# Kernel tuning notes

Measured on AMD Instinct MI355X. Metric: run time of the kernel, lower is better.

The kernel has to match this reference:

```python
import jax, jax.numpy as jnp
from jax import lax
import numpy as np

B, T, H = 128, 512, 512  # batch, seq_length, hidden_dim (== input_dim)


def _xavier(key, shape):
    fan_in, fan_out = shape[1], shape[0]
    limit = float(np.sqrt(6.0 / (fan_in + fan_out)))
    return jax.random.uniform(key, shape, jnp.float32, -limit, limit)


def setup_inputs() -> dict:
    key = jax.random.key(0)
    ks = jax.random.split(key, 10)
    s = 1.0 / np.sqrt(H)  # torch LSTM default init range
    return {
        "x": jax.random.normal(ks[0], (B, T, H), jnp.float32),
        "W_ih": jax.random.uniform(ks[1], (4 * H, H), jnp.float32, -s, s),
        "W_hh": jax.random.uniform(ks[2], (4 * H, H), jnp.float32, -s, s),
        "b_ih": jax.random.uniform(ks[3], (4 * H,), jnp.float32, -s, s),
        "b_hh": jax.random.uniform(ks[4], (4 * H,), jnp.float32, -s, s),
        "Ve": _xavier(ks[5], (1, H)),
        "U1": _xavier(ks[6], (H, 2 * H)),
        "U2": _xavier(ks[7], (H, H)),
        "W_out": _xavier(ks[8], (2, H)),
        "b_out": jnp.zeros((2,), jnp.float32),
    }


def _lstm(x, W_ih, W_hh, b_ih, b_hh):
    # x: [B, T, D] -> hidden states [B, T, H]; PyTorch gate order i,f,g,o
    b = b_ih + b_hh
    # precompute input projections for all timesteps: [T, B, 4H]
    xg = jnp.einsum('btd,gd->tbg', x, W_ih) + b

    def step(carry, xt):
        h, c = carry
        g = xt + h @ W_hh.T  # [B, 4H]
        i, f, gg, o = jnp.split(g, 4, axis=1)
        c = jax.nn.sigmoid(f) * c + jax.nn.sigmoid(i) * jnp.tanh(gg)
        h = jax.nn.sigmoid(o) * jnp.tanh(c)
        return (h, c), h

    h0 = jnp.zeros((x.shape[0], W_hh.shape[1]), x.dtype)
    (_, _), hs = lax.scan(step, (h0, h0), xg)
    return jnp.swapaxes(hs, 0, 1)  # [B, T, H]


def reference(x, W_ih, W_hh, b_ih, b_hh, Ve, U1, U2, W_out, b_out):
    h = _lstm(x, W_ih, W_hh, b_ih, b_hh)  # [B, T, H]
    h_last = h[:, -1, :]  # [B, H]
    # additive attention, vectorized over all timesteps
    Hdim = h.shape[-1]
    u1 = jnp.einsum('bth,gh->btg', h, U1[:, :Hdim]) + jnp.einsum('bh,gh->bg', h_last, U1[:, Hdim:])[:, None, :]
    u2 = jnp.einsum('btd,gd->btg', x, U2)
    u = jnp.tanh(u1 + u2)  # [B, T, H]
    e = jnp.einsum('bth,h->bt', u, Ve[0])
    alpha = jax.nn.softmax(e, axis=1)  # [B, T]
    context = jnp.einsum('bt,bth->bh', alpha, h)  # [B, H]
    params = context @ W_out.T + b_out  # [B, 2]
    mu = params[:, 0]
    sigma = jax.nn.softplus(params[:, 1]) + 1e-5
    return (mu, sigma)
```

## Files before the change

### kernel.cpp

```cpp
#include <hip/hip_runtime.h>
#include <stdint.h>


using short8  = __attribute__((ext_vector_type(8))) short;
using short4v = __attribute__((ext_vector_type(4))) short;
using floatx4 = __attribute__((ext_vector_type(4))) float;

#define MFMA16(a, b, c) __builtin_amdgcn_mfma_f32_16x16x32_bf16((a), (b), (c), 0, 0, 0)

__device__ __forceinline__ unsigned short f2b(float f) {
    unsigned u = __float_as_uint(f);
    u += 0x7FFFu + ((u >> 16) & 1u);
    return (unsigned short)(u >> 16);
}
__device__ __forceinline__ float b2f(unsigned short h) {
    return __uint_as_float(((unsigned)h) << 16);
}
__device__ __forceinline__ float sigm(float x) { return 1.0f / (1.0f + __expf(-x)); }
__device__ __forceinline__ float tanh_(float x) { return 1.0f - 2.0f / (__expf(2.0f * x) + 1.0f); }

__global__ __launch_bounds__(256) void prep(
    const float* __restrict__ x, const float* __restrict__ Wih, const float* __restrict__ Whh,
    const float* __restrict__ bih, const float* __restrict__ bhh,
    const float* __restrict__ U1, const float* __restrict__ U2,
    unsigned short* __restrict__ x_bf, unsigned short* __restrict__ Wih_bf,
    unsigned short* __restrict__ Whh_bf, unsigned short* __restrict__ U1a,
    unsigned short* __restrict__ U1b, unsigned short* __restrict__ U2b,
    float* __restrict__ bias)
{
    const long long NX4 = 33554432LL / 4;
    const long long NREST = 1048576LL + 1048576LL + 524288LL + 262144LL + 2048LL;
    const long long total = NX4 + NREST;
    for (long long u = (long long)blockIdx.x * 256 + threadIdx.x; u < total;
         u += (long long)gridDim.x * 256) {
        if (u < NX4) {
            float4 v = ((const float4*)x)[u];
            short4v o;
            o[0] = (short)f2b(v.x); o[1] = (short)f2b(v.y);
            o[2] = (short)f2b(v.z); o[3] = (short)f2b(v.w);
            *(short4v*)&x_bf[u * 4] = o;
        } else {
            long long i = u - NX4;
            if (i < 1048576) { Wih_bf[i] = f2b(Wih[i]); continue; }
            i -= 1048576;
            if (i < 1048576) { Whh_bf[i] = f2b(Whh[i]); continue; }
            i -= 1048576;
            if (i < 524288) {
                int row = (int)(i >> 10), col = (int)(i & 1023);
                if (col < 512) U1a[row * 512 + col] = f2b(U1[i]);
                else           U1b[row * 512 + (col - 512)] = f2b(U1[i]);
                continue;
            }
            i -= 524288;
            if (i < 262144) { U2b[i] = f2b(U2[i]); continue; }
            i -= 262144;
            bias[i] = bih[i] + bhh[i];
        }
    }
}

__device__ __forceinline__ void gemm_core_t(
    const unsigned short* __restrict__ A, long long lda,
    const unsigned short* __restrict__ Bm,
    unsigned short* __restrict__ C,
    const float* __restrict__ bias,
    int n0, int tfix, int tid, unsigned short* sbuf)
{
    unsigned short* At = sbuf;
    unsigned short* Bt = sbuf + 128 * 72;
    unsigned short* Ct = sbuf;

    const int wv = tid >> 6, lane = tid & 63, l15 = lane & 15, q = lane >> 4;
    const int wm = wv & 1, wn = wv >> 1;

    floatx4 acc[4][4];
    for (int i = 0; i < 4; i++)
        for (int j = 0; j < 4; j++) acc[i][j] = (floatx4){0.f, 0.f, 0.f, 0.f};

    for (int k0 = 0; k0 < 512; k0 += 64) {
        for (int p = 0; p < 4; p++) {
            int idx = tid + p * 256;
            int row = idx >> 3, ch = idx & 7;
            *(short8*)&At[row * 72 + ch * 8] =
                *(const short8*)&A[(long long)row * lda + k0 + ch * 8];
            *(short8*)&Bt[row * 72 + ch * 8] =
                *(const short8*)&Bm[(long long)(n0 + row) * 512 + k0 + ch * 8];
        }
        __syncthreads();
        for (int ks = 0; ks < 64; ks += 32) {
            short8 af[4], bfv[4];
            for (int mi = 0; mi < 4; mi++)
                af[mi] = *(const short8*)&At[(wm * 64 + mi * 16 + l15) * 72 + ks + q * 8];
            for (int ni = 0; ni < 4; ni++)
                bfv[ni] = *(const short8*)&Bt[(wn * 64 + ni * 16 + l15) * 72 + ks + q * 8];
            for (int mi = 0; mi < 4; mi++)
                for (int ni = 0; ni < 4; ni++)
                    acc[mi][ni] = MFMA16(af[mi], bfv[ni], acc[mi][ni]);
        }
        __syncthreads();
    }

    float bv[4];
    for (int ni = 0; ni < 4; ni++)
        bv[ni] = bias[n0 + wn * 64 + ni * 16 + l15];

    for (int mi = 0; mi < 4; mi++)
        for (int ni = 0; ni < 4; ni++)
            for (int r = 0; r < 4; r++)
                Ct[(wm * 64 + mi * 16 + q * 4 + r) * 128 + wn * 64 + ni * 16 + l15] =
                    f2b(acc[mi][ni][r] + bv[ni]);
    __syncthreads();

    for (int p = 0; p < 8; p++) {
        int idx = tid + p * 256;
        int row = idx >> 4, ch = idx & 15;
        int n = n0 + ch * 8;
        int gate = n >> 9, jg = (n >> 4) & 31, c0 = gate * 16 + (n & 15);
        long long dst = (((long long)tfix * 32 + jg) * 128 + row) * 64 + c0;
        *(short8*)&C[dst] = *(const short8*)&Ct[row * 128 + ch * 8];
    }
}

template<int NNI>
__device__ __forceinline__ void attn_helper_body(
    const unsigned short* __restrict__ h_all,
    const unsigned short* __restrict__ x_bf,
    const unsigned short* __restrict__ U1a,
    const unsigned short* __restrict__ U2b,
    unsigned short* __restrict__ xg_out,
    int* __restrict__ syncp,
    int b, int t0, int nBase, int tid, char* smem)
{
    const int bg = b >> 4;
    if (tid < 8) {
        while (__hip_atomic_load(&syncp[16 + (bg * 8 + tid) * 16],
                                 __ATOMIC_RELAXED,
                                 __HIP_MEMORY_SCOPE_AGENT) < t0 + 32)
            __builtin_amdgcn_s_sleep(8);
    }
    __syncthreads();

    unsigned short* Bt2 = (unsigned short*)smem;
    unsigned short* At2 = (unsigned short*)smem + (NNI * 64) * 40;

    const int wv = tid >> 6, lane = tid & 63, l15 = lane & 15, q = lane >> 4;

    floatx4 acc[2][NNI];
    #pragma unroll
    for (int mi = 0; mi < 2; mi++)
        #pragma unroll
        for (int ni = 0; ni < NNI; ni++) acc[mi][ni] = (floatx4){0.f, 0.f, 0.f, 0.f};

    for (int it = 0; it < 32; it++) {
        const int phase = it >> 4, kk = (it & 15) * 32;
        const unsigned short* Bsrc = phase ? U2b : U1a;
        __syncthreads();
        #pragma unroll
        for (int pp = 0; pp < NNI; pp++) {
            int idx = tid + pp * 256;
            int row = idx >> 2, ch = idx & 3;
            *(short8*)&Bt2[row * 40 + ch * 8] =
                *(const short8*)&Bsrc[(long long)(nBase + row) * 512 + kk + ch * 8];
        }
        if (tid < 128) {
            int row = tid >> 2, ch = tid & 3;
            if (phase == 0) {
                unsigned long long* p = (unsigned long long*)
                    &h_all[((long long)b * 512 + t0 + row) * 512 + kk + ch * 8];
                unsigned long long lo = __hip_atomic_load(p, __ATOMIC_RELAXED,
                                                          __HIP_MEMORY_SCOPE_AGENT);
                unsigned long long hi = __hip_atomic_load(p + 1, __ATOMIC_RELAXED,
                                                          __HIP_MEMORY_SCOPE_AGENT);
                unsigned long long* d = (unsigned long long*)&At2[row * 40 + ch * 8];
                d[0] = lo; d[1] = hi;
            } else {
                *(short8*)&At2[row * 40 + ch * 8] =
                    *(const short8*)&x_bf[((long long)b * 512 + t0 + row) * 512 + kk + ch * 8];
            }
        }
        __syncthreads();
        short8 af0 = *(const short8*)&At2[(l15) * 40 + q * 8];
        short8 af1 = *(const short8*)&At2[(16 + l15) * 40 + q * 8];
        #pragma unroll
        for (int ni = 0; ni < NNI; ni++) {
            short8 bfv = *(const short8*)&Bt2[(wv * (NNI * 16) + ni * 16 + l15) * 40 + q * 8];
            acc[0][ni] = MFMA16(af0, bfv, acc[0][ni]);
            acc[1][ni] = MFMA16(af1, bfv, acc[1][ni]);
        }
    }
    #pragma unroll
    for (int mi = 0; mi < 2; mi++)
        #pragma unroll
        for (int ni = 0; ni < NNI; ni++) {
            const int n = nBase + wv * (NNI * 16) + ni * 16 + l15;
            #pragma unroll
            for (int r = 0; r < 4; r++) {
                const int t = t0 + mi * 16 + q * 4 + r;
                float* slot = (float*)&xg_out[(((long long)t * 32 + (n >> 5)) * 128 + b) * 64];
                slot[n & 31] = acc[mi][ni][r];
            }
        }
}

#define GEMM_WGS 8192
#define ATTN_WGS 2432
__global__ __launch_bounds__(256, 1) void mega(
    const unsigned short* __restrict__ xg,
    const unsigned short* __restrict__ Whh,
    unsigned short* __restrict__ h_all,
    unsigned int* __restrict__ ring,
    const unsigned short* __restrict__ x_bf,
    const unsigned short* __restrict__ Wih_bf,
    const float* __restrict__ bias,
    unsigned short* __restrict__ xg_out,
    int* __restrict__ syncp,
    const unsigned short* __restrict__ U1a,
    const unsigned short* __restrict__ U2b)
{
    __shared__ __align__(16) char smem[86016];

    const int tid = threadIdx.x;

    if (blockIdx.x >= 64 && blockIdx.x < 64 + GEMM_WGS) {
        int g = blockIdx.x - 64;
        int t = g >> 4;
        int n0 = (g & 15) << 7;
        gemm_core_t(x_bf + (long long)t * 512, 512LL * 512, Wih_bf,
                    xg_out, bias, n0, t, tid, (unsigned short*)smem);
        __syncthreads();
        if (tid == 0)
            __hip_atomic_fetch_add(&syncp[1088 + t], 1, __ATOMIC_RELEASE,
                                   __HIP_MEMORY_SCOPE_AGENT);
        return;
    }

    if (blockIdx.x >= 64 + GEMM_WGS) {
        const int g = blockIdx.x - 64 - GEMM_WGS;
        if (g < 1920) {
            attn_helper_body<8>(h_all, x_bf, U1a, U2b, xg_out, syncp,
                                g & 127, (g >> 7) * 32, 0, tid, smem);
        } else {
            const int j = g - 1920;
            attn_helper_body<2>(h_all, x_bf, U1a, U2b, xg_out, syncp,
                                j & 127, 480, (j >> 7) * 128, tid, smem);
        }
        return;
    }

    unsigned int (*At)[16 * 264] = (unsigned int (*)[16 * 264])smem;

    const int wv = tid >> 6, lane = tid & 63, l15 = lane & 15, q = lane >> 4;
    const int bg = blockIdx.x >> 3, jgb = blockIdx.x & 7;
    const int b0 = bg * 16;
    const int jg32 = jgb * 4 + wv;
    const int hid = jg32 * 16 + l15;

    short8 Wreg[4][16];
    #pragma unroll
    for (int ct = 0; ct < 4; ct++)
        #pragma unroll
        for (int kk = 0; kk < 16; kk++)
            Wreg[ct][kk] = *(const short8*)
                &Whh[(long long)(ct * 512 + hid) * 512 + kk * 32 + q * 8];

    float cst[4] = {0.f, 0.f, 0.f, 0.f};

    for (int t = 0; t < 512; t++) {
        if ((t & 15) == 0) {
            if (tid < 16) {
                while (__hip_atomic_load(&syncp[1088 + t + tid], __ATOMIC_ACQUIRE,
                                         __HIP_MEMORY_SCOPE_AGENT) < 16)
                    __builtin_amdgcn_s_sleep(8);
            }
            __syncthreads();
        }
        const long long xbase = ((long long)(t * 32 + jg32) * 128 + b0) * 64;
        floatx4 acc[4];
        #pragma unroll
        for (int ct = 0; ct < 4; ct++)
            #pragma unroll
            for (int r = 0; r < 4; r++)
                acc[ct][r] = b2f(xg[xbase + (q * 4 + r) * 64 + ct * 16 + l15]);

        if (t > 0) {
            const unsigned want = (unsigned)(t - 1);
            const int sl = (t - 1) & 1;
            unsigned long long* rb = (unsigned long long*)
                (ring + sl * 65536 + b0 * 512);
            unsigned long long w[16];
            #pragma unroll
            for (int i = 0; i < 16; i++)
                w[i] = __hip_atomic_load(&rb[tid + i * 256], __ATOMIC_RELAXED,
                                         __HIP_MEMORY_SCOPE_AGENT);
            while (true) {
                unsigned bad = 0;
                #pragma unroll
                for (int i = 0; i < 16; i++) {
                    unsigned lo = (unsigned)(w[i] >> 16) & 0xFFFFu;
                    unsigned hi = (unsigned)(w[i] >> 48);
                    bad |= (lo ^ want) | (hi ^ want);
                }
                if (!bad) break;
                #pragma unroll
                for (int i = 0; i < 16; i++) {
                    unsigned lo = (unsigned)(w[i] >> 16) & 0xFFFFu;
                    unsigned hi = (unsigned)(w[i] >> 48);
                    if ((lo ^ want) | (hi ^ want))
                        w[i] = __hip_atomic_load(&rb[tid + i * 256], __ATOMIC_RELAXED,
                                                 __HIP_MEMORY_SCOPE_AGENT);
                }
            }
            unsigned int* dst = &At[sl][0];
            #pragma unroll
            for (int i = 0; i < 16; i++) {
                int idx = tid + i * 256;
                int row = idx >> 8, k = idx & 255;
                dst[row * 264 + k] =
                    (unsigned)(w[i] & 0xFFFFu) | ((unsigned)(w[i] >> 32) << 16);
            }
            __syncthreads();
            const unsigned int* ap = &At[sl][l15 * 264 + q * 4];
            #pragma unroll
            for (int kk = 0; kk < 16; kk++) {
                short8 af = *(const short8*)(ap + kk * 16);
                acc[0] = MFMA16(af, Wreg[0][kk], acc[0]);
                acc[1] = MFMA16(af, Wreg[1][kk], acc[1]);
                acc[2] = MFMA16(af, Wreg[2][kk], acc[2]);
                acc[3] = MFMA16(af, Wreg[3][kk], acc[3]);
            }
        }
        unsigned short hbv[4];
        #pragma unroll
        for (int r = 0; r < 4; r++) {
            float ig = sigm(acc[0][r]);
            float fg = sigm(acc[1][r]);
            float gv = tanh_(acc[2][r]);
            float og = sigm(acc[3][r]);
            cst[r] = fg * cst[r] + ig * gv;
            hbv[r] = f2b(og * tanh_(cst[r]));
        }
        #pragma unroll
        for (int r = 0; r < 4; r++) {
            const int b = b0 + q * 4 + r;
            __hip_atomic_store(&ring[(t & 1) * 65536 + b * 512 + hid],
                               ((unsigned)t << 16) | hbv[r], __ATOMIC_RELAXED,
                               __HIP_MEMORY_SCOPE_AGENT);
        }
        #pragma unroll
        for (int r = 0; r < 4; r++) {
            const int b = b0 + q * 4 + r;
            int o = __shfl_xor((int)hbv[r], 1);
            if (!(l15 & 1)) {
                unsigned v = (unsigned)hbv[r] | (((unsigned)(unsigned short)o) << 16);
                __hip_atomic_store(
                    (unsigned*)&h_all[(long long)b * 262144 + (long long)t * 512 + hid],
                    v, __ATOMIC_RELAXED, __HIP_MEMORY_SCOPE_AGENT);
            }
        }
        if ((t & 15) == 15) {
            __syncthreads();
            if (tid == 0)
                __hip_atomic_store(&syncp[16 + (int)blockIdx.x * 16], t + 1,
                                   __ATOMIC_RELAXED, __HIP_MEMORY_SCOPE_AGENT);
        }
    }
}

__global__ __launch_bounds__(256) void attn_out(
    const unsigned short* __restrict__ a_xg,
    const unsigned short* __restrict__ h_all,
    const unsigned short* __restrict__ U1b,
    const float* __restrict__ Ve,
    const float* __restrict__ Wout, const float* __restrict__ bout,
    float* __restrict__ outp)
{
    __shared__ float hl[512];
    __shared__ float u1s[512];
    __shared__ float se[512];
    __shared__ float sm[512];
    __shared__ float red[8];
    const int b = blockIdx.x, tid = threadIdx.x;
    const int wv = tid >> 6, lane = tid & 63;

    {
        unsigned v = ((const unsigned*)(h_all + (long long)b * 262144 + 511LL * 512))[tid];
        hl[2 * tid]     = b2f((unsigned short)(v & 0xFFFFu));
        hl[2 * tid + 1] = b2f((unsigned short)(v >> 16));
    }
    __syncthreads();
    #pragma unroll
    for (int rr = 0; rr < 2; rr++) {
        const int n = tid + rr * 256;
        const unsigned short* up = &U1b[(long long)n * 512];
        float s = 0.f;
        for (int k = 0; k < 512; k += 8) {
            short8 v8 = *(const short8*)&up[k];
            #pragma unroll
            for (int j = 0; j < 8; j++)
                s += hl[k + j] * b2f((unsigned short)v8[j]);
        }
        u1s[n] = s;
    }
    __syncthreads();

    const int n0 = lane * 8;
    float ve[8], ub[8];
    #pragma unroll
    for (int j = 0; j < 8; j++) {
        ve[j] = Ve[n0 + j];
        ub[j] = u1s[n0 + j];
    }
    for (int it = 0; it < 64; it++) {
        const int t = it * 8 + wv * 2;
        const float* s0p = (const float*)
            &a_xg[(((long long)t * 32 + (n0 >> 5)) * 128 + b) * 64];
        const float* s1p = (const float*)
            &a_xg[(((long long)(t + 1) * 32 + (n0 >> 5)) * 128 + b) * 64];
        float4 a0 = *(const float4*)&s0p[n0 & 31];
        float4 a1 = *(const float4*)&s0p[(n0 & 31) + 4];
        float4 a2 = *(const float4*)&s1p[n0 & 31];
        float4 a3 = *(const float4*)&s1p[(n0 & 31) + 4];
        float s0 = ve[0] * tanh_(a0.x + ub[0]) + ve[1] * tanh_(a0.y + ub[1])
                 + ve[2] * tanh_(a0.z + ub[2]) + ve[3] * tanh_(a0.w + ub[3])
                 + ve[4] * tanh_(a1.x + ub[4]) + ve[5] * tanh_(a1.y + ub[5])
                 + ve[6] * tanh_(a1.z + ub[6]) + ve[7] * tanh_(a1.w + ub[7]);
        float s1 = ve[0] * tanh_(a2.x + ub[0]) + ve[1] * tanh_(a2.y + ub[1])
                 + ve[2] * tanh_(a2.z + ub[2]) + ve[3] * tanh_(a2.w + ub[3])
                 + ve[4] * tanh_(a3.x + ub[4]) + ve[5] * tanh_(a3.y + ub[5])
                 + ve[6] * tanh_(a3.z + ub[6]) + ve[7] * tanh_(a3.w + ub[7]);
        #pragma unroll
        for (int off = 1; off <= 32; off <<= 1) {
            s0 += __shfl_xor(s0, off);
            s1 += __shfl_xor(s1, off);
        }
        if (lane == 0) { se[t] = s0; se[t + 1] = s1; }
    }
    __syncthreads();

    float e0 = se[tid], e1 = se[256 + tid];
    float mx = fmaxf(e0, e1);
    for (int off = 32; off; off >>= 1) mx = fmaxf(mx, __shfl_xor(mx, off));
    if (lane == 0) red[wv] = mx;
    __syncthreads();
    mx = fmaxf(fmaxf(red[0], red[1]), fmaxf(red[2], red[3]));

    float s0 = __expf(e0 - mx), s1 = __expf(e1 - mx);
    sm[tid] = s0; sm[256 + tid] = s1;
    float ss = s0 + s1;
    for (int off = 32; off; off >>= 1) ss += __shfl_xor(ss, off);
    if (lane == 0) red[4 + wv] = ss;
    __syncthreads();
    float inv = 1.0f / (red[4] + red[5] + red[6] + red[7]);

    const unsigned int* hp = (const unsigned int*)(h_all + (long long)b * 262144);
    float a0 = 0.f, a1 = 0.f;
    for (int t = 0; t < 512; t += 4) {
        #pragma unroll
        for (int j = 0; j < 4; j++) {
            float al = sm[t + j];
            unsigned v = hp[(t + j) * 256 + tid];
            a0 += al * b2f((unsigned short)(v & 0xFFFFu));
            a1 += al * b2f((unsigned short)(v >> 16));
        }
    }
    a0 *= inv; a1 *= inv;

    float q0 = a0 * Wout[2 * tid] + a1 * Wout[2 * tid + 1];
    float q1 = a0 * Wout[512 + 2 * tid] + a1 * Wout[512 + 2 * tid + 1];
    for (int off = 32; off; off >>= 1) { q0 += __shfl_xor(q0, off); q1 += __shfl_xor(q1, off); }
    __syncthreads();
    if (lane == 0) { red[wv] = q0; red[4 + wv] = q1; }
    __syncthreads();
    if (tid == 0) {
        float P0 = red[0] + red[1] + red[2] + red[3] + bout[0];
        float P1 = red[4] + red[5] + red[6] + red[7] + bout[1];
        outp[b] = P0;
        float sp = (P1 > 15.0f) ? P1 : log1pf(__expf(P1));
        outp[128 + b] = sp + 1e-5f;
    }
}

extern "C" void kernel_launch(void* const* d_in, const int* in_sizes, int n_in,
                              void* d_out, int out_size, void* d_ws, size_t ws_size,
                              hipStream_t stream)
{
    const float* x    = (const float*)d_in[0];
    const float* Wih  = (const float*)d_in[1];
    const float* Whh  = (const float*)d_in[2];
    const float* bih  = (const float*)d_in[3];
    const float* bhh  = (const float*)d_in[4];
    const float* Ve   = (const float*)d_in[5];
    const float* U1   = (const float*)d_in[6];
    const float* U2   = (const float*)d_in[7];
    const float* Wout = (const float*)d_in[8];
    const float* bout = (const float*)d_in[9];
    float* out = (float*)d_out;

    char* ws = (char*)d_ws;
    size_t off = 0;
    auto alloc = [&](size_t bytes) -> void* {
        void* p = ws + off;
        off += (bytes + 255) & ~(size_t)255;
        return p;
    };
    unsigned short* x_bf   = (unsigned short*)alloc(33554432ull * 2);
    unsigned short* Wih_bf = (unsigned short*)alloc(1048576ull * 2);
    unsigned short* Whh_bf = (unsigned short*)alloc(1048576ull * 2);
    unsigned short* U1a    = (unsigned short*)alloc(262144ull * 2);
    unsigned short* U1b    = (unsigned short*)alloc(262144ull * 2);
    unsigned short* U2b    = (unsigned short*)alloc(262144ull * 2);
    float*          bias   = (float*)alloc(2048ull * 4);
    unsigned short* xg     = (unsigned short*)alloc(134217728ull * 2);
    unsigned short* h_all  = (unsigned short*)alloc(33554432ull * 2);
    unsigned int*   ring   = (unsigned int*)alloc(131072ull * 4);
    int*            syncp  = (int*)alloc(8192ull);
    if (off > ws_size) return;

    hipMemsetAsync(syncp, 0, 8192, stream);
    prep<<<4096, 256, 0, stream>>>(x, Wih, Whh, bih, bhh, U1, U2,
                                   x_bf, Wih_bf, Whh_bf, U1a, U1b, U2b, bias);
    mega<<<64 + GEMM_WGS + ATTN_WGS, 256, 0, stream>>>(
        xg, Whh_bf, h_all, ring, x_bf, Wih_bf, bias, xg, syncp, U1a, U2b);
    attn_out<<<128, 256, 0, stream>>>(xg, h_all, U1b, Ve, Wout, bout, out);
}
```

Measured before the change: 2.645 ms.

## Precompute first input-projection block in separate kernel, coarsen in-kernel GEMM sync

A standalone GEMM kernel now computes the input projection for the first 128 timesteps of every batch before the persistent kernel launches. The in-kernel GEMM workgroups cover only timesteps 128-511, tiled by batch instead of by timestep. The recurrence now waits once, at t=128, on a single global counter instead of polling 16 per-timestep counters every 16 steps. This removes frequent spin-wait synchronization from the serial LSTM loop, at the cost of an extra kernel launch and a serialized prologue GEMM before the recurrence can start.

```diff
diff --git a/kernel.cpp b/kernel.cpp
--- a/kernel.cpp
+++ b/kernel.cpp
@@ -59,12 +59,12 @@
     }
 }
 
-__device__ __forceinline__ void gemm_core_t(
+__device__ __forceinline__ void gemm_core(
     const unsigned short* __restrict__ A, long long lda,
-    const unsigned short* __restrict__ Bm,
-    unsigned short* __restrict__ C,
-    const float* __restrict__ bias,
-    int n0, int tfix, int tid, unsigned short* sbuf)
+    const unsigned short* __restrict__ Bm, long long ldb,
+    unsigned short* __restrict__ C, long long ldc,
+    const float* __restrict__ bias, int mode,
+    int m0, int n0, int tid, unsigned short* sbuf)
 {
     unsigned short* At = sbuf;
     unsigned short* Bt = sbuf + 128 * 72;
@@ -82,9 +82,9 @@
             int idx = tid + p * 256;
             int row = idx >> 3, ch = idx & 7;
             *(short8*)&At[row * 72 + ch * 8] =
-                *(const short8*)&A[(long long)row * lda + k0 + ch * 8];
+                *(const short8*)&A[(long long)(m0 + row) * lda + k0 + ch * 8];
             *(short8*)&Bt[row * 72 + ch * 8] =
-                *(const short8*)&Bm[(long long)(n0 + row) * 512 + k0 + ch * 8];
+                *(const short8*)&Bm[(long long)(n0 + row) * ldb + k0 + ch * 8];
         }
         __syncthreads();
         for (int ks = 0; ks < 64; ks += 32) {
@@ -102,7 +102,7 @@
 
     float bv[4];
     for (int ni = 0; ni < 4; ni++)
-        bv[ni] = bias[n0 + wn * 64 + ni * 16 + l15];
+        bv[ni] = bias ? bias[n0 + wn * 64 + ni * 16 + l15] : 0.0f;
 
     for (int mi = 0; mi < 4; mi++)
         for (int ni = 0; ni < 4; ni++)
@@ -111,14 +111,31 @@
                     f2b(acc[mi][ni][r] + bv[ni]);
     __syncthreads();
 
+    const int tt0 = m0 & 511, bglob = m0 >> 9;
     for (int p = 0; p < 8; p++) {
         int idx = tid + p * 256;
         int row = idx >> 4, ch = idx & 15;
-        int n = n0 + ch * 8;
-        int gate = n >> 9, jg = (n >> 4) & 31, c0 = gate * 16 + (n & 15);
-        long long dst = (((long long)tfix * 32 + jg) * 128 + row) * 64 + c0;
-        *(short8*)&C[dst] = *(const short8*)&Ct[row * 128 + ch * 8];
-    }
+        if (mode) {
+            int n = n0 + ch * 8;
+            int gate = n >> 9, jg = (n >> 4) & 31, c0 = gate * 16 + (n & 15);
+            long long dst = (((long long)(tt0 + row) * 32 + jg) * 128 + bglob) * 64 + c0;
+            *(short8*)&C[dst] = *(const short8*)&Ct[row * 128 + ch * 8];
+        } else {
+            *(short8*)&C[(long long)(m0 + row) * ldc + n0 + ch * 8] =
+                *(const short8*)&Ct[row * 128 + ch * 8];
+        }
+    }
+}
+
+__global__ __launch_bounds__(256) void gemm_bt(
+    const unsigned short* __restrict__ A, long long lda,
+    const unsigned short* __restrict__ Bm, long long ldb,
+    unsigned short* __restrict__ C, long long ldc,
+    const float* __restrict__ bias, int mode, int mmul)
+{
+    __shared__ __align__(16) unsigned short sbuf[2 * 128 * 72];
+    gemm_core(A, lda, Bm, ldb, C, ldc, bias, mode,
+              blockIdx.x * mmul, blockIdx.y * 128, threadIdx.x, sbuf);
 }
 
 template<int NNI>
@@ -202,7 +219,7 @@
         }
 }
 
-#define GEMM_WGS 8192
+#define GEMM_WGS 6144
 #define ATTN_WGS 2432
 __global__ __launch_bounds__(256, 1) void mega(
     const unsigned short* __restrict__ xg,
@@ -223,13 +240,15 @@
 
     if (blockIdx.x >= 64 && blockIdx.x < 64 + GEMM_WGS) {
         int g = blockIdx.x - 64;
-        int t = g >> 4;
-        int n0 = (g & 15) << 7;
-        gemm_core_t(x_bf + (long long)t * 512, 512LL * 512, Wih_bf,
-                    xg_out, bias, n0, t, tid, (unsigned short*)smem);
+        int b = g & 127;
+        int r = g >> 7;
+        int ti = 1 + (r % 3);
+        int n = r / 3;
+        gemm_core(x_bf, 512, Wih_bf, 512, xg_out, 2048, bias, 1,
+                  b * 512 + ti * 128, n * 128, tid, (unsigned short*)smem);
         __syncthreads();
         if (tid == 0)
-            __hip_atomic_fetch_add(&syncp[1088 + t], 1, __ATOMIC_RELEASE,
+            __hip_atomic_fetch_add(&syncp[0], 1, __ATOMIC_RELEASE,
                                    __HIP_MEMORY_SCOPE_AGENT);
         return;
     }
@@ -266,10 +285,10 @@
     float cst[4] = {0.f, 0.f, 0.f, 0.f};
 
     for (int t = 0; t < 512; t++) {
-        if ((t & 15) == 0) {
-            if (tid < 16) {
-                while (__hip_atomic_load(&syncp[1088 + t + tid], __ATOMIC_ACQUIRE,
-                                         __HIP_MEMORY_SCOPE_AGENT) < 16)
+        if (t == 128) {
+            if (tid == 0) {
+                while (__hip_atomic_load(&syncp[0], __ATOMIC_ACQUIRE,
+                                         __HIP_MEMORY_SCOPE_AGENT) < GEMM_WGS)
                     __builtin_amdgcn_s_sleep(8);
             }
             __syncthreads();
@@ -519,6 +538,8 @@
     hipMemsetAsync(syncp, 0, 8192, stream);
     prep<<<4096, 256, 0, stream>>>(x, Wih, Whh, bih, bhh, U1, U2,
                                    x_bf, Wih_bf, Whh_bf, U1a, U1b, U2b, bias);
+    gemm_bt<<<dim3(128, 16), 256, 0, stream>>>(x_bf, 512, Wih_bf, 512,
+                                               xg, 2048, bias, 1, 512);
     mega<<<64 + GEMM_WGS + ATTN_WGS, 256, 0, stream>>>(
         xg, Whh_bf, h_all, ring, x_bf, Wih_bf, bias, xg, syncp, U1a, U2b);
     attn_out<<<128, 256, 0, stream>>>(xg, h_all, U1b, Ve, Wout, bout, out);
```

After: 2.567 ms. -2.9%, faster.
